# Optimization experiments

Hardware: AMD Instinct MI355X
Metric: run time of the kernel (lower is better)

## Reference

```python
import jax, jax.numpy as jnp
import numpy as np

N_NODES = 150000
N_EDGES = 300000
N_LG_EDGES = 600000
N_TREE = 60000
HIDDEN = 256
DEPTH = 4
ATOM_FDIM = 35
BOND_FDIM = 5
NUM_GRAPHS = 2048


def setup_inputs() -> dict:
    key = jax.random.key(0)
    ks = jax.random.split(key, 14)
    return {
        "node_x": jax.random.normal(ks[0], (N_NODES, ATOM_FDIM), dtype=jnp.float32),
        "bond_x": jax.random.normal(ks[1], (N_EDGES, BOND_FDIM), dtype=jnp.float32),
        "tree_mess": jax.random.normal(ks[2], (N_TREE, HIDDEN), dtype=jnp.float32),
        "W_i": jax.random.normal(ks[3], (ATOM_FDIM + BOND_FDIM, HIDDEN), dtype=jnp.float32) * 0.05,
        "W_h": jax.random.normal(ks[4], (HIDDEN, HIDDEN), dtype=jnp.float32) * 0.05,
        "W_o": jax.random.normal(ks[5], (ATOM_FDIM + HIDDEN, HIDDEN), dtype=jnp.float32) * 0.05,
        "b_o": jax.random.normal(ks[6], (HIDDEN,), dtype=jnp.float32) * 0.05,
        "edge_src": jax.random.randint(ks[7], (N_EDGES,), 0, N_NODES, dtype=jnp.int64 if jax.config.jax_enable_x64 else jnp.int32).astype(jnp.int32),
        "edge_dst": jax.random.randint(ks[8], (N_EDGES,), 0, N_NODES).astype(jnp.int32),
        "lg_src": jax.random.randint(ks[9], (N_LG_EDGES,), 0, N_EDGES).astype(jnp.int32),
        "lg_dst": jax.random.randint(ks[10], (N_LG_EDGES,), 0, N_EDGES).astype(jnp.int32),
        "tgt_nodes": jax.random.randint(ks[11], (N_TREE,), 0, N_NODES).astype(jnp.int32),
        "graph_ids": jnp.sort(jax.random.randint(ks[12], (N_NODES,), 0, NUM_GRAPHS)).astype(jnp.int32),
        "num_graphs": NUM_GRAPHS,
    }


def reference(node_x, bond_x, tree_mess, W_i, W_h, W_o, b_o,
              edge_src, edge_dst, lg_src, lg_dst, tgt_nodes, graph_ids, num_graphs):
    n_nodes = node_x.shape[0]
    n_edges = bond_x.shape[0]

    # msg_input = W_i([src_atom_x ; bond_x])  (no bias)
    features = jnp.concatenate([node_x[edge_src], bond_x], axis=1)  # [E, 40]
    msg_input = features @ W_i                                       # [E, H]
    msg = jax.nn.relu(msg_input)

    # tree-message alpha: scatter_add tree messages onto target atoms (non-PAPER branch)
    node_alpha = jnp.zeros((n_nodes, msg.shape[1]), msg.dtype).at[tgt_nodes].add(tree_mess)
    edge_alpha = node_alpha[edge_src]  # apply_edges: alpha = src['alpha']

    # loopy BP on the line graph: accum = sum of incoming line-graph messages
    def body(msg, _):
        accum = jax.ops.segment_sum(msg[lg_src], lg_dst, num_segments=n_edges)
        msg = jax.nn.relu(msg_input + (accum + edge_alpha) @ W_h)
        return msg, None

    msg, _ = jax.lax.scan(body, msg, None, length=DEPTH - 1)

    # gather: m[v] = sum of msg over incoming edges; h = relu(W_o([x ; m + alpha]) + b)
    m = jax.ops.segment_sum(msg, edge_dst, num_segments=n_nodes)
    h = jax.nn.relu(jnp.concatenate([node_x, m + node_alpha], axis=1) @ W_o + b_o)

    # mean_nodes per graph
    counts = jax.ops.segment_sum(jnp.ones((n_nodes,), h.dtype), graph_ids, num_segments=num_graphs)
    g_sum = jax.ops.segment_sum(h, graph_ids, num_segments=num_graphs)
    g_repr = g_sum / jnp.maximum(counts, 1.0)[:, None]
    return g_repr
```

## Files before the change

kernel.cpp:

```cpp
#include <hip/hip_runtime.h>
#include <stdint.h>

#define HID 256
#define CAP 16

typedef __attribute__((ext_vector_type(8))) short bf16x8;
typedef __attribute__((ext_vector_type(4))) float f32x4;
typedef __attribute__((ext_vector_type(2))) float f32x2;

__device__ __forceinline__ float bf2f(unsigned short u) {
    union { unsigned int i; float f; } v; v.i = ((unsigned int)u) << 16; return v.f;
}
__device__ __forceinline__ unsigned short f2bf(float f) {
    union { float f; unsigned int i; } v; v.f = f;
    unsigned int r = (v.i + 0x7fffu + ((v.i >> 16) & 1u)) >> 16;
    return (unsigned short)r;
}
__device__ __forceinline__ float fp82f_sw(unsigned char b) {
    unsigned int s = (unsigned int)(b & 0x80) << 24;
    int e = (b >> 3) & 0xF;
    int m = b & 7;
    float v;
    if (e) v = __uint_as_float(((unsigned int)(e + 120) << 23) | ((unsigned int)m << 20));
    else   v = (float)m * 0.001953125f;
    return __uint_as_float(__float_as_uint(v) | s);
}
__device__ __forceinline__ unsigned char f2fp8_sw(float x) {
    unsigned int bits = __float_as_uint(x);
    unsigned char s = (unsigned char)((bits >> 24) & 0x80);
    float ax = fabsf(x);
    if (!(ax >= 0.001953125f)) {
        int n = (int)rintf(ax * 512.f);
        return s | (unsigned char)n;
    }
    if (ax >= 448.f) return s | 0x7E;
    int ex; float mant = frexpf(ax, &ex);
    int e = ex + 6;
    if (e >= 1) {
        int q = (int)rintf(mant * 16.f);
        if (q == 16) { q = 8; ++e; }
        if (e > 15 || (e == 15 && q > 14)) return s | 0x7E;
        return s | (unsigned char)((e << 3) | (q - 8));
    } else {
        int n = (int)rintf(ax * 512.f);
        if (n >= 8) return s | 0x08;
        return s | (unsigned char)n;
    }
}
__device__ __forceinline__ unsigned char f2fp8(float x) {
#if __has_builtin(__builtin_amdgcn_cvt_pk_fp8_f32)
    return (unsigned char)(__builtin_amdgcn_cvt_pk_fp8_f32(x, x, 0, false) & 0xff);
#else
    return f2fp8_sw(x);
#endif
}
__device__ __forceinline__ f32x4 fp8x4_to_f32(unsigned int u) {
#if __has_builtin(__builtin_amdgcn_cvt_pk_f32_fp8)
    f32x2 a = __builtin_amdgcn_cvt_pk_f32_fp8(u, false);
    f32x2 b = __builtin_amdgcn_cvt_pk_f32_fp8(u, true);
    f32x4 r; r[0] = a.x; r[1] = a.y; r[2] = b.x; r[3] = b.y;
    return r;
#else
    f32x4 r;
    #pragma unroll
    for (int q = 0; q < 4; ++q) r[q] = fp82f_sw((u >> (8 * q)) & 0xff);
    return r;
#endif
}
__device__ __forceinline__ bf16x8 fp8x8_to_bf16x8(uint2 raw) {
#if __has_builtin(__builtin_amdgcn_cvt_pk_f32_fp8)
    f32x2 p0 = __builtin_amdgcn_cvt_pk_f32_fp8(raw.x, false);
    f32x2 p1 = __builtin_amdgcn_cvt_pk_f32_fp8(raw.x, true);
    f32x2 p2 = __builtin_amdgcn_cvt_pk_f32_fp8(raw.y, false);
    f32x2 p3 = __builtin_amdgcn_cvt_pk_f32_fp8(raw.y, true);
    union { unsigned int u[4]; bf16x8 v; } cv;
    cv.u[0] = (__float_as_uint(p0.x) >> 16) | (__float_as_uint(p0.y) & 0xffff0000u);
    cv.u[1] = (__float_as_uint(p1.x) >> 16) | (__float_as_uint(p1.y) & 0xffff0000u);
    cv.u[2] = (__float_as_uint(p2.x) >> 16) | (__float_as_uint(p2.y) & 0xffff0000u);
    cv.u[3] = (__float_as_uint(p3.x) >> 16) | (__float_as_uint(p3.y) & 0xffff0000u);
    return cv.v;
#else
    union { unsigned short u[8]; bf16x8 v; } cv;
    #pragma unroll
    for (int q = 0; q < 4; ++q) cv.u[q]     = f2bf(fp82f_sw((raw.x >> (8 * q)) & 0xff));
    #pragma unroll
    for (int q = 0; q < 4; ++q) cv.u[4 + q] = f2bf(fp82f_sw((raw.y >> (8 * q)) & 0xff));
    return cv.v;
#endif
}

__device__ __forceinline__ void llds16(const void* g, void* l) {
    __builtin_amdgcn_global_load_lds(
        (const __attribute__((address_space(1))) void*)g,
        (__attribute__((address_space(3))) void*)l, 16, 0, 0);
}


__global__ void k_zero_f(float* __restrict__ p, size_t n) {
    size_t i = (size_t)blockIdx.x * 256 + threadIdx.x;
    if (i < n) p[i] = 0.f;
}
__global__ void k_diag(float* __restrict__ out, float v) {
    if (blockIdx.x == 0 && threadIdx.x == 0) out[0] = v;
}

__global__ void k_init(int* __restrict__ cnt_lg, int E,
                       int* __restrict__ cnt_nd, int* __restrict__ cnt_t, int N,
                       int* __restrict__ gcnt, int* __restrict__ gstart, int G) {
    int i = blockIdx.x * 256 + threadIdx.x;
    if (i < E) cnt_lg[i] = 0;
    if (i < N) { cnt_nd[i] = 0; cnt_t[i] = 0; }
    if (i < G) { gcnt[i] = 0; gstart[i] = N; }
}

__global__ void k_alpha(const float* __restrict__ tm, const int* __restrict__ cnt,
                        const int* __restrict__ bkt, unsigned char* __restrict__ alpha, int N) {
    int wave = threadIdx.x >> 6, lane = threadIdx.x & 63;
    int v = blockIdx.x * 4 + wave;
    if (v >= N) return;
    int d = cnt[v]; if (d > CAP) d = CAP;
    f32x4 s = {0.f, 0.f, 0.f, 0.f};
    const int* bb = bkt + (size_t)v * CAP;
    for (int t = 0; t < d; ++t) {
        int r = bb[t];
        f32x4 x = *(const f32x4*)(tm + (size_t)r * HID + lane * 4);
        #pragma unroll
        for (int k = 0; k < 4; ++k) s[k] += x[k];
    }
    union { unsigned char b[4]; unsigned int u; } ov;
    #pragma unroll
    for (int k = 0; k < 4; ++k) ov.b[k] = f2fp8(s[k]);
    *(unsigned int*)(alpha + (size_t)v * HID + lane * 4) = ov.u;
}

__global__ void k_wt_i(const float* __restrict__ W, unsigned short* __restrict__ Wt) {
    int i = blockIdx.x * 256 + threadIdx.x;
    int n = i >> 6, k = i & 63;
    Wt[i] = f2bf((k < 40) ? W[k * HID + n] : 0.f);
}
__global__ void k_wt_hi(const float* __restrict__ Wh, const float* __restrict__ Wi,
                        unsigned short* __restrict__ Wt) {
    int i = blockIdx.x * 256 + threadIdx.x;
    int n = i / 320, k = i % 320;
    float v;
    if (k < 256) v = Wh[(size_t)k * HID + n];
    else if (k < 296) v = Wi[(size_t)(k - 256) * HID + n];
    else v = 0.f;
    Wt[i] = f2bf(v);
}
__global__ void k_wt_o(const float* __restrict__ W, unsigned short* __restrict__ Wt) {
    int i = blockIdx.x * 256 + threadIdx.x;
    int n = i / 320, k = i % 320;
    float v;
    if (k < 256) v = W[(size_t)(35 + k) * HID + n];
    else if (k < 291) v = W[(size_t)(k - 256) * HID + n];
    else v = 0.f;
    Wt[i] = f2bf(v);
}

__global__ void k_a1(const float* __restrict__ nx, const float* __restrict__ bx,
                     const int* __restrict__ esrc, unsigned char* __restrict__ A1, int E) {
    int i = blockIdx.x * 256 + threadIdx.x;
    if (i >= E * 64) return;
    int e = i >> 6, k = i & 63;
    float v = 0.f;
    if (k < 35) v = nx[(size_t)esrc[e] * 35 + k];
    else if (k < 40) v = bx[(size_t)e * 5 + (k - 35)];
    A1[i] = f2fp8(v);
}

__global__ void k_x1(const float* __restrict__ nx, unsigned char* __restrict__ X1, int N) {
    int i = blockIdx.x * 256 + threadIdx.x;
    if (i >= N * 64) return;
    int v = i >> 6, k = i & 63;
    X1[i] = f2fp8((k < 35) ? nx[(size_t)v * 35 + k] : 0.f);
}

__global__ void k_fill(const int* __restrict__ dst, const int* __restrict__ val,
                       int* __restrict__ cnt, int* __restrict__ bkt, int n, int useval) {
    int i = blockIdx.x * 256 + threadIdx.x;
    if (i >= n) return;
    int d = dst[i];
    int p = atomicAdd(&cnt[d], 1);
    if (p < CAP) bkt[(size_t)d * CAP + p] = useval ? val[i] : i;
}

__global__ void k_gfill(const int* __restrict__ gid, int* __restrict__ gstart,
                        int* __restrict__ gcnt, int N) {
    int i = blockIdx.x * 256 + threadIdx.x;
    if (i >= N) return;
    int g = gid[i];
    atomicAdd(&gcnt[g], 1);
    atomicMin(&gstart[g], i);
}

template<int BN, int K1, int KTOT, int EPI, bool PF8, bool QF8, bool OUTF8>
__global__ __launch_bounds__(256, 2)
void gemm5(const void* __restrict__ Ap, int lda1,
           const void* __restrict__ Aq, int lda2,
           const unsigned short* __restrict__ B, int M,
           void* __restrict__ out, const float* __restrict__ bias)
{
    constexpr int NKC = KTOT / 64;
    constexpr int NB  = (NKC > 1) ? 2 : 1;
    constexpr bool ABF = (K1 > 0 && !PF8) || (KTOT > K1 && !QF8);
    constexpr int ASZ = ABF ? 128 * 128 : 128 * 64;
    constexpr int BSZ = BN * 128;
    constexpr int JN  = BN / 32;
    __shared__ unsigned char Als[NB * ASZ];
    __shared__ unsigned char Bls[NB * BSZ];
    const int tid  = threadIdx.x;
    const int lane = tid & 63;
    const int wid  = tid >> 6;
    const int wm = wid & 1, wn = wid >> 1;
    const int row0 = blockIdx.x * 128;
    const int colb = blockIdx.y * BN;
    const int l15  = lane & 15;
    const int quad = lane >> 4;

    f32x4 acc[4][JN] = {};

    const int sA8_r = lane >> 2, sA8_c = lane & 3;
    const int s16_r = lane >> 3, s16_c = lane & 7;

    auto stageA = [&](int kc, int bb) {
        const bool pPart = (kc * 64 < K1);
        const void* As = pPart ? Ap : Aq;
        const int  lda  = pPart ? lda1 : lda2;
        const int  kofs = pPart ? kc * 64 : kc * 64 - K1;
        const bool f8   = pPart ? PF8 : QF8;
        if (f8) {
            #pragma unroll
            for (int t = 0; t < 2; ++t) {
                int r = wid * 32 + t * 16 + sA8_r;
                int ar = row0 + r; if (ar > M - 1) ar = M - 1;
                int ck = sA8_c ^ (r & 3);
                const unsigned char* g = (const unsigned char*)As + (size_t)ar * lda + kofs + ck * 16;
                llds16(g, &Als[bb + (wid * 32 + t * 16) * 64]);
            }
        } else {
            #pragma unroll
            for (int t = 0; t < 4; ++t) {
                int r = wid * 32 + t * 8 + s16_r;
                int ar = row0 + r; if (ar > M - 1) ar = M - 1;
                int ck = s16_c ^ (r & 7);
                const unsigned char* g = (const unsigned char*)As + ((size_t)ar * lda + kofs) * 2 + ck * 16;
                llds16(g, &Als[bb + (wid * 32 + t * 8) * 128]);
            }
        }
    };
    auto stageB = [&](int kc, int bb) {
        #pragma unroll
        for (int t = 0; t < BN / 32; ++t) {
            int r = wid * (BN / 4) + t * 8 + s16_r;
            int ck = s16_c ^ (r & 7);
            const unsigned char* g = (const unsigned char*)B + ((size_t)(colb + r) * KTOT + kc * 64) * 2 + ck * 16;
            llds16(g, &Bls[bb + (wid * (BN / 4) + t * 8) * 128]);
        }
    };

    stageA(0, 0);
    stageB(0, 0);
    int cur = 0;
    #pragma unroll
    for (int kc = 0; kc < NKC; ++kc) {
        __syncthreads();
        if (kc + 1 < NKC) { stageA(kc + 1, (cur ^ 1) * ASZ); stageB(kc + 1, (cur ^ 1) * BSZ); }
        const bool f8 = (kc * 64 < K1) ? PF8 : QF8;
        const int abase = cur * ASZ, bbase = cur * BSZ;
        #pragma unroll
        for (int kk = 0; kk < 64; kk += 32) {
            bf16x8 af[4];
            #pragma unroll
            for (int i = 0; i < 4; ++i) {
                int arow = wm * 64 + i * 16 + l15;
                if (f8) {
                    int ck = (kk >> 4) + (quad >> 1);
                    uint2 raw = *(const uint2*)&Als[abase + arow * 64 + ((ck ^ (arow & 3)) << 4) + ((quad & 1) << 3)];
                    af[i] = fp8x8_to_bf16x8(raw);
                } else {
                    int ck = (kk >> 3) + quad;
                    af[i] = *(const bf16x8*)&Als[abase + arow * 128 + ((ck ^ (arow & 7)) << 4)];
                }
            }
            #pragma unroll
            for (int j = 0; j < JN; ++j) {
                int brow = wn * (BN / 2) + j * 16 + l15;
                int ck = (kk >> 3) + quad;
                bf16x8 bfr = *(const bf16x8*)&Bls[bbase + brow * 128 + ((ck ^ (brow & 7)) << 4)];
                #pragma unroll
                for (int i = 0; i < 4; ++i)
                    acc[i][j] = __builtin_amdgcn_mfma_f32_16x16x32_bf16(af[i], bfr, acc[i][j], 0, 0, 0);
            }
        }
        cur ^= 1;
    }

    #pragma unroll
    for (int i = 0; i < 4; ++i) {
        int rbase = row0 + wm * 64 + i * 16 + quad * 4;
        #pragma unroll
        for (int r = 0; r < 4; ++r) {
            int row = rbase + r;
            if (row >= M) continue;
            #pragma unroll
            for (int j = 0; j < JN; ++j) {
                int col = colb + wn * (BN / 2) + j * 16 + l15;
                float v = acc[i][j][r];
                if (EPI == 1) v += bias[col];
                v = v > 0.f ? v : 0.f;
                if (OUTF8) ((unsigned char*)out)[(size_t)row * HID + col] = f2fp8(v);
                else       ((unsigned short*)out)[(size_t)row * HID + col] = f2bf(v);
            }
        }
    }
}


__global__ void k_accum(const unsigned char* __restrict__ msg, const unsigned char* __restrict__ alpha,
                        const int* __restrict__ esrc, const int* __restrict__ cnt,
                        const int* __restrict__ bkt, unsigned char* __restrict__ accum, int E)
{
    int tid  = threadIdx.x;
    int lane = tid & 63, wave = tid >> 6;
    int sub  = lane >> 4;
    int sl   = lane & 15;
    int e = blockIdx.x * 16 + wave * 4 + sub;
    if (e >= E) return;
    int c = sl * 16;
    int src = esrc[e];
    int d = cnt[e]; if (d > CAP) d = CAP;
    uint4 au = *(const uint4*)(alpha + (size_t)src * HID + c);
    f32x4 s0 = fp8x4_to_f32(au.x);
    f32x4 s1 = fp8x4_to_f32(au.y);
    f32x4 s2 = fp8x4_to_f32(au.z);
    f32x4 s3 = fp8x4_to_f32(au.w);
    const int* bb = bkt + (size_t)e * CAP;
    for (int base = 0; base < d; base += 4) {
        int4 bi = *(const int4*)(bb + base);
        int rem = d - base;
        int i0 = bi.x;
        int i1 = (rem > 1) ? bi.y : bi.x;
        int i2 = (rem > 2) ? bi.z : bi.x;
        int i3 = (rem > 3) ? bi.w : bi.x;
        uint4 m0 = *(const uint4*)(msg + (size_t)i0 * HID + c);
        uint4 m1 = *(const uint4*)(msg + (size_t)i1 * HID + c);
        uint4 m2 = *(const uint4*)(msg + (size_t)i2 * HID + c);
        uint4 m3 = *(const uint4*)(msg + (size_t)i3 * HID + c);
        {   f32x4 a0 = fp8x4_to_f32(m0.x), a1 = fp8x4_to_f32(m0.y), a2 = fp8x4_to_f32(m0.z), a3 = fp8x4_to_f32(m0.w);
            #pragma unroll
            for (int k = 0; k < 4; ++k) { s0[k] += a0[k]; s1[k] += a1[k]; s2[k] += a2[k]; s3[k] += a3[k]; } }
        if (rem > 1) { f32x4 a0 = fp8x4_to_f32(m1.x), a1 = fp8x4_to_f32(m1.y), a2 = fp8x4_to_f32(m1.z), a3 = fp8x4_to_f32(m1.w);
            #pragma unroll
            for (int k = 0; k < 4; ++k) { s0[k] += a0[k]; s1[k] += a1[k]; s2[k] += a2[k]; s3[k] += a3[k]; } }
        if (rem > 2) { f32x4 a0 = fp8x4_to_f32(m2.x), a1 = fp8x4_to_f32(m2.y), a2 = fp8x4_to_f32(m2.z), a3 = fp8x4_to_f32(m2.w);
            #pragma unroll
            for (int k = 0; k < 4; ++k) { s0[k] += a0[k]; s1[k] += a1[k]; s2[k] += a2[k]; s3[k] += a3[k]; } }
        if (rem > 3) { f32x4 a0 = fp8x4_to_f32(m3.x), a1 = fp8x4_to_f32(m3.y), a2 = fp8x4_to_f32(m3.z), a3 = fp8x4_to_f32(m3.w);
            #pragma unroll
            for (int k = 0; k < 4; ++k) { s0[k] += a0[k]; s1[k] += a1[k]; s2[k] += a2[k]; s3[k] += a3[k]; } }
    }
    union { unsigned char b[16]; uint4 u; } ov;
    #pragma unroll
    for (int k = 0; k < 4; ++k) {
        ov.b[k]      = f2fp8(s0[k]);
        ov.b[4 + k]  = f2fp8(s1[k]);
        ov.b[8 + k]  = f2fp8(s2[k]);
        ov.b[12 + k] = f2fp8(s3[k]);
    }
    *(uint4*)(accum + (size_t)e * HID + c) = ov.u;
}

__global__ void k_mpa(const unsigned char* __restrict__ msg, const unsigned char* __restrict__ alpha,
                      const int* __restrict__ cnt, const int* __restrict__ bkt,
                      unsigned short* __restrict__ Mb, int N)
{
    int wave = threadIdx.x >> 6;
    int lane = threadIdx.x & 63;
    int sub  = lane >> 5;
    int sl   = lane & 31;
    int v = blockIdx.x * 8 + wave * 2 + sub;
    if (v >= N) return;
    int c = sl * 8;
    int d = cnt[v]; if (d > CAP) d = CAP;
    uint2 au = *(const uint2*)(alpha + (size_t)v * HID + c);
    f32x4 s0 = fp8x4_to_f32(au.x);
    f32x4 s1 = fp8x4_to_f32(au.y);
    const int* bb = bkt + (size_t)v * CAP;
    for (int base = 0; base < d; base += 4) {
        int4 bi = *(const int4*)(bb + base);
        int rem = d - base;
        int i0 = bi.x;
        int i1 = (rem > 1) ? bi.y : bi.x;
        int i2 = (rem > 2) ? bi.z : bi.x;
        int i3 = (rem > 3) ? bi.w : bi.x;
        uint2 m0 = *(const uint2*)(msg + (size_t)i0 * HID + c);
        uint2 m1 = *(const uint2*)(msg + (size_t)i1 * HID + c);
        uint2 m2 = *(const uint2*)(msg + (size_t)i2 * HID + c);
        uint2 m3 = *(const uint2*)(msg + (size_t)i3 * HID + c);
        {   f32x4 vx = fp8x4_to_f32(m0.x), vy = fp8x4_to_f32(m0.y);
            #pragma unroll
            for (int k = 0; k < 4; ++k) { s0[k] += vx[k]; s1[k] += vy[k]; } }
        if (rem > 1) { f32x4 vx = fp8x4_to_f32(m1.x), vy = fp8x4_to_f32(m1.y);
            #pragma unroll
            for (int k = 0; k < 4; ++k) { s0[k] += vx[k]; s1[k] += vy[k]; } }
        if (rem > 2) { f32x4 vx = fp8x4_to_f32(m2.x), vy = fp8x4_to_f32(m2.y);
            #pragma unroll
            for (int k = 0; k < 4; ++k) { s0[k] += vx[k]; s1[k] += vy[k]; } }
        if (rem > 3) { f32x4 vx = fp8x4_to_f32(m3.x), vy = fp8x4_to_f32(m3.y);
            #pragma unroll
            for (int k = 0; k < 4; ++k) { s0[k] += vx[k]; s1[k] += vy[k]; } }
    }
    union { unsigned short h[8]; uint4 u; } ov;
    #pragma unroll
    for (int k = 0; k < 4; ++k) { ov.h[k] = f2bf(s0[k]); ov.h[4 + k] = f2bf(s1[k]); }
    *(uint4*)(Mb + (size_t)v * HID + c) = ov.u;
}

__global__ void k_gmean(const unsigned short* __restrict__ h, const int* __restrict__ gstart,
                        const int* __restrict__ gcnt, float* __restrict__ out, int G) {
    int g = blockIdx.x;
    int c = threadIdx.x;
    int st = gstart[g], n = gcnt[g];
    float s = 0.f;
    for (int r = 0; r < n; ++r) s += bf2f(h[(size_t)(st + r) * HID + c]);
    out[(size_t)g * HID + c] = (n > 0) ? s / (float)n : 0.f;
}

extern "C" void kernel_launch(void* const* d_in, const int* in_sizes, int n_in,
                              void* d_out, int out_size, void* d_ws, size_t ws_size,
                              hipStream_t stream)
{
    const float* node_x    = (const float*)d_in[0];
    const float* bond_x    = (const float*)d_in[1];
    const float* tree_mess = (const float*)d_in[2];
    const float* W_i       = (const float*)d_in[3];
    const float* W_h       = (const float*)d_in[4];
    const float* W_o       = (const float*)d_in[5];
    const float* b_o       = (const float*)d_in[6];
    const int* edge_src    = (const int*)d_in[7];
    const int* edge_dst    = (const int*)d_in[8];
    const int* lg_src      = (const int*)d_in[9];
    const int* lg_dst      = (const int*)d_in[10];
    const int* tgt_nodes   = (const int*)d_in[11];
    const int* graph_ids   = (const int*)d_in[12];

    const int N = in_sizes[0] / 35;
    const int E = in_sizes[1] / 5;
    const int T = in_sizes[2] / HID;
    const int L = in_sizes[9];
    const int G = out_size / HID;

    auto rup = [](size_t b) { return (b + 255) & ~(size_t)255; };
    const size_t szAcc = (size_t)E * HID;
    const size_t szMsg = (size_t)E * HID;
    const size_t szMbN = (size_t)N * HID * 2;
    const size_t R_acc = rup(szAcc > szMbN ? szAcc : szMbN);
    const size_t R_msg = rup(szMsg > szMbN ? szMsg : szMbN);
    const size_t R_al  = rup((size_t)N * HID);
    const size_t R_a1  = rup((size_t)E * 64);
    const size_t need = R_acc + R_msg + R_al + R_a1
        + rup(256 * 64 * 2) + rup((size_t)256 * 320 * 2) * 2
        + rup((size_t)E * 4) + rup((size_t)E * CAP * 4)
        + rup((size_t)N * 4) + rup((size_t)N * CAP * 4)
        + rup((size_t)N * 4) + rup((size_t)N * CAP * 4)
        + rup((size_t)G * 4) * 2;

    if (need > ws_size) {
        k_zero_f<<<(out_size + 255) / 256, 256, 0, stream>>>((float*)d_out, (size_t)out_size);
        k_diag<<<1, 64, 0, stream>>>((float*)d_out, (float)(ws_size >> 20));
        return;
    }

    char* w = (char*)d_ws;
    auto alloc = [&](size_t bytes) { char* p = w; w += (bytes + 255) & ~(size_t)255; return p; };
    char* r_acc = (char*)alloc(R_acc);
    char* r_msg = (char*)alloc(R_msg);
    char* r_al  = (char*)alloc(R_al);
    char* r_a1  = (char*)alloc(R_a1);
    unsigned short* Wt_i  = (unsigned short*)alloc(256 * 64 * 2);
    unsigned short* Wt_hi = (unsigned short*)alloc((size_t)256 * 320 * 2);
    unsigned short* Wt_o  = (unsigned short*)alloc((size_t)256 * 320 * 2);
    int* cnt_lg = (int*)alloc((size_t)E * 4);
    int* bkt_lg = (int*)alloc((size_t)E * CAP * 4);
    int* cnt_nd = (int*)alloc((size_t)N * 4);
    int* bkt_nd = (int*)alloc((size_t)N * CAP * 4);
    int* cnt_t  = (int*)alloc((size_t)N * 4);
    int* bkt_t  = (int*)alloc((size_t)N * CAP * 4);
    int* gstart = (int*)alloc((size_t)G * 4);
    int* gcnt   = (int*)alloc((size_t)G * 4);

    unsigned char*  accum = (unsigned char*)r_acc;
    unsigned short* Mb    = (unsigned short*)r_acc;
    unsigned char*  msg   = (unsigned char*)r_msg;
    unsigned short* h     = (unsigned short*)r_msg;
    unsigned char*  alpha = (unsigned char*)r_al;
    unsigned char*  A1    = (unsigned char*)r_a1;
    unsigned char*  X1    = (unsigned char*)r_a1;

    k_init<<<(E + 255) / 256, 256, 0, stream>>>(cnt_lg, E, cnt_nd, cnt_t, N, gcnt, gstart, G);

    k_wt_i<<<64, 256, 0, stream>>>(W_i, Wt_i);
    k_wt_hi<<<320, 256, 0, stream>>>(W_h, W_i, Wt_hi);
    k_wt_o<<<320, 256, 0, stream>>>(W_o, Wt_o);
    k_fill<<<(L + 255) / 256, 256, 0, stream>>>(lg_dst, lg_src, cnt_lg, bkt_lg, L, 1);
    k_fill<<<(E + 255) / 256, 256, 0, stream>>>(edge_dst, (const int*)nullptr, cnt_nd, bkt_nd, E, 0);
    k_fill<<<(T + 255) / 256, 256, 0, stream>>>(tgt_nodes, (const int*)nullptr, cnt_t, bkt_t, T, 0);
    k_gfill<<<(N + 255) / 256, 256, 0, stream>>>(graph_ids, gstart, gcnt, N);
    k_alpha<<<(N + 3) / 4, 256, 0, stream>>>(tree_mess, cnt_t, bkt_t, alpha, N);
    k_a1<<<(E * 64 + 255) / 256, 256, 0, stream>>>(node_x, bond_x, edge_src, A1, E);

    dim3 gE((E + 127) / 128, 1), gN((N + 127) / 128, 2);

    gemm5<256, 0, 64, 0, false, true, true><<<gE, 256, 0, stream>>>(nullptr, 0, A1, 64, Wt_i, E, msg, nullptr);

    for (int it = 0; it < 3; ++it) {
        k_accum<<<(E + 15) / 16, 256, 0, stream>>>(msg, alpha, edge_src, cnt_lg, bkt_lg, accum, E);
        gemm5<256, 256, 320, 0, true, true, true><<<gE, 256, 0, stream>>>(accum, 256, A1, 64, Wt_hi, E, msg, nullptr);
    }

    k_x1<<<(N * 64 + 255) / 256, 256, 0, stream>>>(node_x, X1, N);
    k_mpa<<<(N + 7) / 8, 256, 0, stream>>>(msg, alpha, cnt_nd, bkt_nd, Mb, N);
    gemm5<128, 256, 320, 1, false, true, false><<<gN, 256, 0, stream>>>(Mb, 256, X1, 64, Wt_o, N, h, b_o);
    k_gmean<<<G, 256, 0, stream>>>(h, gstart, gcnt, (float*)d_out, G);
}
```

Measured before the change: 868.7 us.

## Pre-permute weights into MFMA fragment order and read B directly from global

The transposed weight tables are stored in a segmented layout that matches the MFMA B-fragment order. The GEMM can then load B fragments straight from global memory, where they are expected to stay in L2, instead of staging them through LDS. The A operand is now loaded for all K chunks up front with a single barrier, replacing the double-buffered pipeline. Every block also computes all 256 output columns, which changes the output GEMM from a 2-column-block grid to one. The cost is a larger accumulator footprint, which may hurt occupancy, and global-latency-bound B loads with no overlap of A loads.

New measurement: 946.1 us. +8.9%, slower.

```diff
diff --git a/kernel.cpp b/kernel.cpp
--- a/kernel.cpp
+++ b/kernel.cpp
@@ -133,29 +133,33 @@
     *(unsigned int*)(alpha + (size_t)v * HID + lane * 4) = ov.u;
 }
 
+
 __global__ void k_wt_i(const float* __restrict__ W, unsigned short* __restrict__ Wt) {
-    int i = blockIdx.x * 256 + threadIdx.x;
-    int n = i >> 6, k = i & 63;
-    Wt[i] = f2bf((k < 40) ? W[k * HID + n] : 0.f);
+    int o = blockIdx.x * 256 + threadIdx.x;
+    int seg = o >> 11, n = (o >> 3) & 255, b = o & 7;
+    int k = (seg >> 3) * 64 + ((seg >> 2) & 1) * 32 + (seg & 3) * 8 + b;
+    Wt[o] = f2bf((k < 40) ? W[k * HID + n] : 0.f);
 }
 __global__ void k_wt_hi(const float* __restrict__ Wh, const float* __restrict__ Wi,
                         unsigned short* __restrict__ Wt) {
-    int i = blockIdx.x * 256 + threadIdx.x;
-    int n = i / 320, k = i % 320;
+    int o = blockIdx.x * 256 + threadIdx.x;
+    int seg = o >> 11, n = (o >> 3) & 255, b = o & 7;
+    int k = (seg >> 3) * 64 + ((seg >> 2) & 1) * 32 + (seg & 3) * 8 + b;
     float v;
     if (k < 256) v = Wh[(size_t)k * HID + n];
     else if (k < 296) v = Wi[(size_t)(k - 256) * HID + n];
     else v = 0.f;
-    Wt[i] = f2bf(v);
+    Wt[o] = f2bf(v);
 }
 __global__ void k_wt_o(const float* __restrict__ W, unsigned short* __restrict__ Wt) {
-    int i = blockIdx.x * 256 + threadIdx.x;
-    int n = i / 320, k = i % 320;
+    int o = blockIdx.x * 256 + threadIdx.x;
+    int seg = o >> 11, n = (o >> 3) & 255, b = o & 7;
+    int k = (seg >> 3) * 64 + ((seg >> 2) & 1) * 32 + (seg & 3) * 8 + b;
     float v;
     if (k < 256) v = W[(size_t)(35 + k) * HID + n];
     else if (k < 291) v = W[(size_t)(k - 256) * HID + n];
     else v = 0.f;
-    Wt[i] = f2bf(v);
+    Wt[o] = f2bf(v);
 }
 
 __global__ void k_a1(const float* __restrict__ nx, const float* __restrict__ bx,
@@ -194,40 +198,39 @@
     atomicMin(&gstart[g], i);
 }
 
-template<int BN, int K1, int KTOT, int EPI, bool PF8, bool QF8, bool OUTF8>
+template<int K1, int KTOT, int EPI, bool PF8, bool QF8, bool OUTF8>
 __global__ __launch_bounds__(256, 2)
-void gemm5(const void* __restrict__ Ap, int lda1,
+void gemm6(const void* __restrict__ Ap, int lda1,
            const void* __restrict__ Aq, int lda2,
            const unsigned short* __restrict__ B, int M,
            void* __restrict__ out, const float* __restrict__ bias)
 {
     constexpr int NKC = KTOT / 64;
-    constexpr int NB  = (NKC > 1) ? 2 : 1;
-    constexpr bool ABF = (K1 > 0 && !PF8) || (KTOT > K1 && !QF8);
-    constexpr int ASZ = ABF ? 128 * 128 : 128 * 64;
-    constexpr int BSZ = BN * 128;
-    constexpr int JN  = BN / 32;
-    __shared__ unsigned char Als[NB * ASZ];
-    __shared__ unsigned char Bls[NB * BSZ];
+    constexpr int NK1 = K1 / 64;
+    constexpr int R1  = PF8 ? 64 : 128;
+    constexpr int R2  = QF8 ? 64 : 128;
+    constexpr int ATOT = NK1 * 128 * R1 + (NKC - NK1) * 128 * R2;
+    __shared__ unsigned char Als[ATOT];
     const int tid  = threadIdx.x;
     const int lane = tid & 63;
     const int wid  = tid >> 6;
     const int wm = wid & 1, wn = wid >> 1;
     const int row0 = blockIdx.x * 128;
-    const int colb = blockIdx.y * BN;
     const int l15  = lane & 15;
     const int quad = lane >> 4;
 
-    f32x4 acc[4][JN] = {};
+    f32x4 acc[4][8] = {};
 
     const int sA8_r = lane >> 2, sA8_c = lane & 3;
     const int s16_r = lane >> 3, s16_c = lane & 7;
 
-    auto stageA = [&](int kc, int bb) {
-        const bool pPart = (kc * 64 < K1);
+    #pragma unroll
+    for (int kc = 0; kc < NKC; ++kc) {
+        const bool pPart = (kc < NK1);
         const void* As = pPart ? Ap : Aq;
         const int  lda  = pPart ? lda1 : lda2;
-        const int  kofs = pPart ? kc * 64 : kc * 64 - K1;
+        const int  kofs = pPart ? kc * 64 : (kc - NK1) * 64;
+        const int  aoff = pPart ? kc * 128 * R1 : NK1 * 128 * R1 + (kc - NK1) * 128 * R2;
         const bool f8   = pPart ? PF8 : QF8;
         if (f8) {
             #pragma unroll
@@ -236,7 +239,7 @@
                 int ar = row0 + r; if (ar > M - 1) ar = M - 1;
                 int ck = sA8_c ^ (r & 3);
                 const unsigned char* g = (const unsigned char*)As + (size_t)ar * lda + kofs + ck * 16;
-                llds16(g, &Als[bb + (wid * 32 + t * 16) * 64]);
+                llds16(g, &Als[aoff + (wid * 32 + t * 16) * 64]);
             }
         } else {
             #pragma unroll
@@ -245,29 +248,16 @@
                 int ar = row0 + r; if (ar > M - 1) ar = M - 1;
                 int ck = s16_c ^ (r & 7);
                 const unsigned char* g = (const unsigned char*)As + ((size_t)ar * lda + kofs) * 2 + ck * 16;
-                llds16(g, &Als[bb + (wid * 32 + t * 8) * 128]);
+                llds16(g, &Als[aoff + (wid * 32 + t * 8) * 128]);
             }
         }
-    };
-    auto stageB = [&](int kc, int bb) {
-        #pragma unroll
-        for (int t = 0; t < BN / 32; ++t) {
-            int r = wid * (BN / 4) + t * 8 + s16_r;
-            int ck = s16_c ^ (r & 7);
-            const unsigned char* g = (const unsigned char*)B + ((size_t)(colb + r) * KTOT + kc * 64) * 2 + ck * 16;
-            llds16(g, &Bls[bb + (wid * (BN / 4) + t * 8) * 128]);
-        }
-    };
-
-    stageA(0, 0);
-    stageB(0, 0);
-    int cur = 0;
+    }
+    __syncthreads();
+
     #pragma unroll
     for (int kc = 0; kc < NKC; ++kc) {
-        __syncthreads();
-        if (kc + 1 < NKC) { stageA(kc + 1, (cur ^ 1) * ASZ); stageB(kc + 1, (cur ^ 1) * BSZ); }
-        const bool f8 = (kc * 64 < K1) ? PF8 : QF8;
-        const int abase = cur * ASZ, bbase = cur * BSZ;
+        const bool f8  = (kc < NK1) ? PF8 : QF8;
+        const int aoff = (kc < NK1) ? kc * 128 * R1 : NK1 * 128 * R1 + (kc - NK1) * 128 * R2;
         #pragma unroll
         for (int kk = 0; kk < 64; kk += 32) {
             bf16x8 af[4];
@@ -276,24 +266,23 @@
                 int arow = wm * 64 + i * 16 + l15;
                 if (f8) {
                     int ck = (kk >> 4) + (quad >> 1);
-                    uint2 raw = *(const uint2*)&Als[abase + arow * 64 + ((ck ^ (arow & 3)) << 4) + ((quad & 1) << 3)];
+                    uint2 raw = *(const uint2*)&Als[aoff + arow * 64 + ((ck ^ (arow & 3)) << 4) + ((quad & 1) << 3)];
                     af[i] = fp8x8_to_bf16x8(raw);
                 } else {
                     int ck = (kk >> 3) + quad;
-                    af[i] = *(const bf16x8*)&Als[abase + arow * 128 + ((ck ^ (arow & 7)) << 4)];
+                    af[i] = *(const bf16x8*)&Als[aoff + arow * 128 + ((ck ^ (arow & 7)) << 4)];
                 }
             }
-            #pragma unroll
-            for (int j = 0; j < JN; ++j) {
-                int brow = wn * (BN / 2) + j * 16 + l15;
-                int ck = (kk >> 3) + quad;
-                bf16x8 bfr = *(const bf16x8*)&Bls[bbase + brow * 128 + ((ck ^ (brow & 7)) << 4)];
+            const int seg = (kc * 2 + (kk >> 5)) * 4 + quad;
+            const bf16x8* bp = (const bf16x8*)(B + (size_t)seg * 2048);
+            #pragma unroll
+            for (int j = 0; j < 8; ++j) {
+                bf16x8 bfr = bp[wn * 128 + j * 16 + l15];
                 #pragma unroll
                 for (int i = 0; i < 4; ++i)
                     acc[i][j] = __builtin_amdgcn_mfma_f32_16x16x32_bf16(af[i], bfr, acc[i][j], 0, 0, 0);
             }
         }
-        cur ^= 1;
     }
 
     #pragma unroll
@@ -304,8 +293,8 @@
             int row = rbase + r;
             if (row >= M) continue;
             #pragma unroll
-            for (int j = 0; j < JN; ++j) {
-                int col = colb + wn * (BN / 2) + j * 16 + l15;
+            for (int j = 0; j < 8; ++j) {
+                int col = wn * 128 + j * 16 + l15;
                 float v = acc[i][j][r];
                 if (EPI == 1) v += bias[col];
                 v = v > 0.f ? v : 0.f;
@@ -510,17 +499,17 @@
     k_alpha<<<(N + 3) / 4, 256, 0, stream>>>(tree_mess, cnt_t, bkt_t, alpha, N);
     k_a1<<<(E * 64 + 255) / 256, 256, 0, stream>>>(node_x, bond_x, edge_src, A1, E);
 
-    dim3 gE((E + 127) / 128, 1), gN((N + 127) / 128, 2);
-
-    gemm5<256, 0, 64, 0, false, true, true><<<gE, 256, 0, stream>>>(nullptr, 0, A1, 64, Wt_i, E, msg, nullptr);
+    dim3 gE((E + 127) / 128, 1), gN((N + 127) / 128, 1);
+
+    gemm6<0, 64, 0, false, true, true><<<gE, 256, 0, stream>>>(nullptr, 0, A1, 64, Wt_i, E, msg, nullptr);
 
     for (int it = 0; it < 3; ++it) {
         k_accum<<<(E + 15) / 16, 256, 0, stream>>>(msg, alpha, edge_src, cnt_lg, bkt_lg, accum, E);
-        gemm5<256, 256, 320, 0, true, true, true><<<gE, 256, 0, stream>>>(accum, 256, A1, 64, Wt_hi, E, msg, nullptr);
+        gemm6<256, 320, 0, true, true, true><<<gE, 256, 0, stream>>>(accum, 256, A1, 64, Wt_hi, E, msg, nullptr);
     }
 
     k_x1<<<(N * 64 + 255) / 256, 256, 0, stream>>>(node_x, X1, N);
     k_mpa<<<(N + 7) / 8, 256, 0, stream>>>(msg, alpha, cnt_nd, bkt_nd, Mb, N);
-    gemm5<128, 256, 320, 1, false, true, false><<<gN, 256, 0, stream>>>(Mb, 256, X1, 64, Wt_o, N, h, b_o);
+    gemm6<256, 320, 1, false, true, false><<<gN, 256, 0, stream>>>(Mb, 256, X1, 64, Wt_o, N, h, b_o);
     k_gmean<<<G, 256, 0, stream>>>(h, gstart, gcnt, (float*)d_out, G);
 }
```
